# Optimization experiments

Measured on AMD Instinct MI355X. Metric: run time of the kernel, lower is better.

Reference implementation:

```python
import jax, jax.numpy as jnp
import numpy as np

N_WAY = 100
K_SHOT = 10
N_SUPPORT = N_WAY * K_SHOT
N_QUERY = 8192
F_IN = 4096
D_EMB = 1024
EPS = 1e-6  # torch nn.PairwiseDistance default eps added to the difference


def setup_inputs() -> dict:
    key = jax.random.key(0)
    k1, k2, k3, k4 = jax.random.split(key, 4)
    support_images = jax.random.normal(k1, (N_SUPPORT, F_IN), dtype=jnp.float32)
    # dense labels 0..N_WAY-1, K_SHOT examples each (episodic sampling)
    support_labels = (jnp.arange(N_SUPPORT, dtype=jnp.int32) // K_SHOT)
    query_images = jax.random.normal(k2, (N_QUERY, F_IN), dtype=jnp.float32)
    W = jax.random.normal(k3, (F_IN, D_EMB), dtype=jnp.float32) * (1.0 / np.sqrt(F_IN))
    b = jax.random.normal(k4, (D_EMB,), dtype=jnp.float32) * 0.01
    return {"support_images": support_images, "support_labels": support_labels,
            "query_images": query_images, "W": W, "b": b}


def reference(support_images, support_labels, query_images, W, b):
    # backbone: linear feature extractor
    z_support = support_images @ W + b          # [N_SUPPORT, D]
    z_query = query_images @ W + b              # [N_QUERY, D]

    # group support embeddings by class (each class has exactly K_SHOT members)
    order = jnp.argsort(support_labels, stable=True)
    grouped = z_support[order].reshape(N_WAY, K_SHOT, D_EMB)  # [W, K, D]

    # torch .median(dim=0): lower median for even counts -> sorted[(K-1)//2]
    z_proto_med = jnp.sort(grouped, axis=1)[:, (K_SHOT - 1) // 2]  # [W, D]
    z_proto_mean = grouped.mean(axis=1)                            # [W, D]
    z_total = 0.5 * (z_proto_med + z_proto_mean)                   # [W, D]

    # pairwise L2 with torch PairwiseDistance eps: sqrt(sum((q - p + eps)^2))
    # expanded: ||q||^2 + ||p||^2 + D*eps^2 - 2 q.p + 2*eps*(sum q - sum p)
    q2 = jnp.sum(z_query * z_query, axis=-1, keepdims=True)       # [Q, 1]
    p2 = jnp.sum(z_total * z_total, axis=-1)[None, :]             # [1, W]
    qs = jnp.sum(z_query, axis=-1, keepdims=True)                 # [Q, 1]
    ps = jnp.sum(z_total, axis=-1)[None, :]                       # [1, W]
    cross = z_query @ z_total.T                                   # [Q, W]
    sq = q2 + p2 - 2.0 * cross + 2.0 * EPS * (qs - ps) + D_EMB * EPS * EPS
    dists = jnp.sqrt(jnp.maximum(sq, 0.0))                        # [Q, W]
    return -dists
```

## Files before the change

### kernel.cpp

```cpp
#include <hip/hip_runtime.h>


typedef unsigned short u16;
typedef __attribute__((ext_vector_type(4))) unsigned short u16x4;
typedef __attribute__((ext_vector_type(8))) unsigned short u16x8;
typedef __attribute__((ext_vector_type(8))) short bf16x8;
typedef __attribute__((ext_vector_type(4))) float f32x4;

#define N_QUERY 8192
#define F_IN    4096
#define D_EMB   1024
#define N_SUP   1000
#define N_WAY   100
#define BK      64

__device__ __forceinline__ u16 f2b(float f) {
  unsigned int u = __builtin_bit_cast(unsigned int, f);
  u += 0x7FFFu + ((u >> 16) & 1u);
  return (u16)(u >> 16);
}

#define GLB_PTR(p) ((const __attribute__((address_space(1))) unsigned int*)(p))
#define LDS_PTR(p) ((__attribute__((address_space(3))) unsigned int*)(p))

__global__ __launch_bounds__(256) void wt_k(const float* __restrict__ W,
                                            u16* __restrict__ Wt) {
  __shared__ float tile[32][33];
  int kb = blockIdx.x * 32, nb = blockIdx.y * 32;
  int tx = threadIdx.x & 31, ty = threadIdx.x >> 5;
#pragma unroll
  for (int i = 0; i < 4; ++i) {
    int k = ty + i * 8;
    tile[k][tx] = W[(size_t)(kb + k) * D_EMB + nb + tx];
  }
  __syncthreads();
#pragma unroll
  for (int i = 0; i < 4; ++i) {
    int n = ty + i * 8;
    Wt[(size_t)(nb + n) * F_IN + kb + tx] = f2b(tile[tx][n]);
  }
}

__global__ __launch_bounds__(256) void gemm1_k(
    const float* __restrict__ qimg, const float* __restrict__ simg,
    const u16* __restrict__ Wt, const float* __restrict__ bias,
    float* __restrict__ Z) {
  __shared__ __align__(16) u16 As[64 * BK];
  __shared__ __align__(16) u16 Bs[128 * BK];
  const int tid  = threadIdx.x;
  const int lane = tid & 63, wid = tid >> 6;
  const int wr = wid >> 1, wc = wid & 1;
  int lin = blockIdx.x + (blockIdx.y << 3);
  int swz = (lin & 7) * 144 + (lin >> 3);
  const int rowBase = (swz >> 3) * 64;
  const int colBase = (swz & 7) * 128;

  const float* asrc[2];
  int aw[2];
#pragma unroll
  for (int i = 0; i < 2; ++i) {
    int g = i * 256 + tid;
    int row = g >> 3;
    int colb = ((g & 7) << 4) ^ ((row & 7) << 4);
    int grow = rowBase + row;
    int sr = grow - N_QUERY; if (sr < 0) sr = 0; if (sr > N_SUP - 1) sr = N_SUP - 1;
    const float* base = (grow < N_QUERY) ? qimg + (size_t)grow * F_IN
                                         : simg + (size_t)sr * F_IN;
    asrc[i] = base + (colb >> 1);
    aw[i] = g * 8;
  }
  const u16* bsrc[4];
  unsigned bldsoff[4];
#pragma unroll
  for (int i = 0; i < 4; ++i) {
    int g = i * 256 + tid;
    int n = g >> 3;
    int kb = ((g & 7) << 4) ^ ((n & 7) << 4);
    bsrc[i] = Wt + (size_t)(colBase + n) * F_IN + (kb >> 1);
    bldsoff[i] = i * 4096 + wid * 1024;
  }
  int aoff[2], boff[4];
#pragma unroll
  for (int m = 0; m < 2; ++m) {
    int row = wr * 32 + m * 16 + (lane & 15);
    aoff[m] = (row * 128 + (((lane >> 4) << 4) ^ ((row & 7) << 4))) >> 1;
  }
#pragma unroll
  for (int n = 0; n < 4; ++n) {
    int row = wc * 64 + n * 16 + (lane & 15);
    boff[n] = (row * 128 + (((lane >> 4) << 4) ^ ((row & 7) << 4))) >> 1;
  }

  f32x4 acc[2][4] = {};

#pragma unroll 1
  for (int kt = 0; kt < F_IN / BK; ++kt) {
    const float* p0 = asrc[0] + kt * BK;
    const float* p1 = asrc[1] + kt * BK;
    float4 v00 = *(const float4*)p0, v01 = *(const float4*)(p0 + 4);
    float4 v10 = *(const float4*)p1, v11 = *(const float4*)(p1 + 4);
#pragma unroll
    for (int i = 0; i < 4; ++i)
      __builtin_amdgcn_global_load_lds(GLB_PTR(bsrc[i] + kt * BK),
                                       LDS_PTR((char*)Bs + bldsoff[i]), 16, 0, 0);
    u16x8 pk0 = { f2b(v00.x), f2b(v00.y), f2b(v00.z), f2b(v00.w),
                  f2b(v01.x), f2b(v01.y), f2b(v01.z), f2b(v01.w) };
    u16x8 pk1 = { f2b(v10.x), f2b(v10.y), f2b(v10.z), f2b(v10.w),
                  f2b(v11.x), f2b(v11.y), f2b(v11.z), f2b(v11.w) };
    *(u16x8*)&As[aw[0]] = pk0;
    *(u16x8*)&As[aw[1]] = pk1;
    __syncthreads();

#pragma unroll
    for (int ks = 0; ks < 2; ++ks) {
      bf16x8 a[2], b[4];
#pragma unroll
      for (int m = 0; m < 2; ++m) a[m] = *(const bf16x8*)&As[aoff[m] ^ (ks << 5)];
#pragma unroll
      for (int n = 0; n < 4; ++n) b[n] = *(const bf16x8*)&Bs[boff[n] ^ (ks << 5)];
#pragma unroll
      for (int m = 0; m < 2; ++m)
#pragma unroll
        for (int n = 0; n < 4; ++n)
          acc[m][n] = __builtin_amdgcn_mfma_f32_16x16x32_bf16(a[m], b[n], acc[m][n], 0, 0, 0);
    }
    __syncthreads();
  }

#pragma unroll
  for (int n = 0; n < 4; ++n) {
    int c = colBase + wc * 64 + n * 16 + (lane & 15);
    float bvv = bias[c];
#pragma unroll
    for (int m = 0; m < 2; ++m) {
      int r0 = rowBase + wr * 32 + m * 16 + ((lane >> 4) * 4);
#pragma unroll
      for (int r = 0; r < 4; ++r)
        Z[(size_t)(r0 + r) * D_EMB + c] = acc[m][n][r] + bvv;
    }
  }
}

__global__ __launch_bounds__(256) void proto_k(const float* __restrict__ Z,
                                               float* __restrict__ Ztf) {
  int gid = blockIdx.x * 256 + threadIdx.x;
  int w = gid >> 10, d = gid & 1023;
  float outv = 0.f;
  if (w < N_WAY) {
    float v[10]; float s = 0.f;
#pragma unroll
    for (int k = 0; k < 10; ++k) {
      v[k] = Z[(size_t)(N_QUERY + w * 10 + k) * D_EMB + d];
      s += v[k];
    }
#pragma unroll
    for (int a = 0; a < 9; ++a)
#pragma unroll
      for (int b2 = 0; b2 < 9; ++b2)
        if (b2 < 9 - a) {
          float lo = fminf(v[b2], v[b2 + 1]);
          float hi = fmaxf(v[b2], v[b2 + 1]);
          v[b2] = lo; v[b2 + 1] = hi;
        }
    outv = 0.5f * (v[4] + s * 0.1f);
  }
  Ztf[gid] = outv;
}

__global__ __launch_bounds__(256) void stats_k(const float* __restrict__ in,
                                               u16* __restrict__ outb,
                                               float* __restrict__ sum2,
                                               float* __restrict__ sum1) {
  int row = blockIdx.x;
  const float* r = in + (size_t)row * D_EMB;
  int t = threadIdx.x;
  float4 v = *(const float4*)(r + t * 4);
  u16x4 u4 = { f2b(v.x), f2b(v.y), f2b(v.z), f2b(v.w) };
  *(u16x4*)(outb + (size_t)row * D_EMB + t * 4) = u4;
  float s  = v.x + v.y + v.z + v.w;
  float s2 = v.x * v.x + v.y * v.y + v.z * v.z + v.w * v.w;
#pragma unroll
  for (int off = 32; off > 0; off >>= 1) {
    s  += __shfl_down(s, off);
    s2 += __shfl_down(s2, off);
  }
  __shared__ float as1[4], as2[4];
  if ((t & 63) == 0) { as1[t >> 6] = s; as2[t >> 6] = s2; }
  __syncthreads();
  if (t == 0) {
    sum1[row] = as1[0] + as1[1] + as1[2] + as1[3];
    sum2[row] = as2[0] + as2[1] + as2[2] + as2[3];
  }
}

#define LDA2 40
__global__ __launch_bounds__(256) void gemm2_k(
    const u16* __restrict__ Zq, const u16* __restrict__ Ztb,
    const float* __restrict__ q2, const float* __restrict__ qs,
    const float* __restrict__ p2, const float* __restrict__ ps,
    float* __restrict__ out) {
  __shared__ u16 As[64][LDA2];
  __shared__ u16 Bs[128][LDA2];
  const int tid = threadIdx.x;
  const int lane = tid & 63, wid = tid >> 6;
  const int wr = wid >> 1, wc = wid & 1;
  const int rowBase = blockIdx.x * 64;

  f32x4 acc[2][4] = {};

  for (int kt = 0; kt < D_EMB / 32; ++kt) {
    u16x8 avv;
    {
      int row = tid >> 2, kh = tid & 3;
      avv = *(const u16x8*)(Zq + (size_t)(rowBase + row) * D_EMB + kt * 32 + kh * 8);
    }
    u16x8 bvv[2];
#pragma unroll
    for (int i = 0; i < 2; ++i) {
      int u = i * 256 + tid;
      int n = u >> 2, kh = u & 3;
      bvv[i] = *(const u16x8*)(Ztb + (size_t)n * D_EMB + kt * 32 + kh * 8);
    }
    __syncthreads();
    {
      int row = tid >> 2, kh = tid & 3;
      *(u16x8*)&As[row][kh * 8] = avv;
    }
#pragma unroll
    for (int i = 0; i < 2; ++i) {
      int u = i * 256 + tid;
      int n = u >> 2, kh = u & 3;
      *(u16x8*)&Bs[n][kh * 8] = bvv[i];
    }
    __syncthreads();

    bf16x8 a[2], b[4];
#pragma unroll
    for (int m = 0; m < 2; ++m)
      a[m] = *(const bf16x8*)&As[wr * 32 + m * 16 + (lane & 15)][(lane >> 4) * 8];
#pragma unroll
    for (int n = 0; n < 4; ++n)
      b[n] = *(const bf16x8*)&Bs[wc * 64 + n * 16 + (lane & 15)][(lane >> 4) * 8];
#pragma unroll
    for (int m = 0; m < 2; ++m)
#pragma unroll
      for (int n = 0; n < 4; ++n)
        acc[m][n] = __builtin_amdgcn_mfma_f32_16x16x32_bf16(a[m], b[n], acc[m][n], 0, 0, 0);
    __syncthreads();
  }

#pragma unroll
  for (int m = 0; m < 2; ++m) {
    int r0 = rowBase + wr * 32 + m * 16 + ((lane >> 4) * 4);
    float q2v[4], qsv[4];
#pragma unroll
    for (int r = 0; r < 4; ++r) { q2v[r] = q2[r0 + r]; qsv[r] = qs[r0 + r]; }
#pragma unroll
    for (int n = 0; n < 4; ++n) {
      int c = wc * 64 + n * 16 + (lane & 15);
      if (c < N_WAY) {
        float pp = p2[c], pss = ps[c];
#pragma unroll
        for (int r = 0; r < 4; ++r) {
          float sq = q2v[r] + pp - 2.f * acc[m][n][r]
                   + 2e-6f * (qsv[r] - pss) + (float)D_EMB * 1e-12f;
          out[(size_t)(r0 + r) * N_WAY + c] = -sqrtf(fmaxf(sq, 0.f));
        }
      }
    }
  }
}

extern "C" void kernel_launch(void* const* d_in, const int* in_sizes, int n_in,
                              void* d_out, int out_size, void* d_ws, size_t ws_size,
                              hipStream_t stream) {
  const float* simg = (const float*)d_in[0];
  const float* qimg = (const float*)d_in[2];
  const float* W    = (const float*)d_in[3];
  const float* bias = (const float*)d_in[4];
  float* out = (float*)d_out;

  char* ws = (char*)d_ws;
  u16*   Wt  = (u16*)(ws);
  float* Z   = (float*)(ws + 8388608);
  u16*   Zq  = (u16*)(ws + 46137344);
  float* Ztf = (float*)(ws + 62914560);
  u16*   Ztb = (u16*)(ws + 63438848);
  float* q2  = (float*)(ws + 63700992);
  float* qs  = (float*)(ws + 63733760);
  float* p2  = (float*)(ws + 63766528);
  float* ps  = (float*)(ws + 63767040);

  hipLaunchKernelGGL(wt_k,    dim3(128, 32), dim3(256), 0, stream, W, Wt);
  hipLaunchKernelGGL(gemm1_k, dim3(8, 144),  dim3(256), 0, stream, qimg, simg, Wt, bias, Z);
  hipLaunchKernelGGL(proto_k, dim3(512),     dim3(256), 0, stream, Z, Ztf);
  hipLaunchKernelGGL(stats_k, dim3(8192),    dim3(256), 0, stream, Z, Zq, q2, qs);
  hipLaunchKernelGGL(stats_k, dim3(128),     dim3(256), 0, stream, Ztf, Ztb, p2, ps);
  hipLaunchKernelGGL(gemm2_k, dim3(128),     dim3(256), 0, stream, Zq, Ztb, q2, qs, p2, ps, out);
}
```

Baseline: 170.4 us.

## Split GEMM1 K-loop across two warp groups with LDS reduction

```diff
diff --git a/kernel.cpp b/kernel.cpp
--- a/kernel.cpp
+++ b/kernel.cpp
@@ -41,25 +41,29 @@
   }
 }
 
-__global__ __launch_bounds__(256) void gemm1_k(
+__global__ __launch_bounds__(512, 6) void gemm1_k(
     const float* __restrict__ qimg, const float* __restrict__ simg,
     const u16* __restrict__ Wt, const float* __restrict__ bias,
     float* __restrict__ Z) {
-  __shared__ __align__(16) u16 As[64 * BK];
-  __shared__ __align__(16) u16 Bs[128 * BK];
+  __shared__ __align__(16) u16 ldsAll[2][(64 + 128) * BK];
   const int tid  = threadIdx.x;
   const int lane = tid & 63, wid = tid >> 6;
-  const int wr = wid >> 1, wc = wid & 1;
+  const int grp  = wid >> 2, lwid = wid & 3;
+  const int gtid = tid & 255;
+  const int wr = lwid >> 1, wc = lwid & 1;
+  u16* As = &ldsAll[grp][0];
+  u16* Bs = &ldsAll[grp][64 * BK];
   int lin = blockIdx.x + (blockIdx.y << 3);
   int swz = (lin & 7) * 144 + (lin >> 3);
   const int rowBase = (swz >> 3) * 64;
   const int colBase = (swz & 7) * 128;
+  const int kt0 = grp << 5;
 
   const float* asrc[2];
   int aw[2];
 #pragma unroll
   for (int i = 0; i < 2; ++i) {
-    int g = i * 256 + tid;
+    int g = i * 256 + gtid;
     int row = g >> 3;
     int colb = ((g & 7) << 4) ^ ((row & 7) << 4);
     int grow = rowBase + row;
@@ -73,11 +77,11 @@
   unsigned bldsoff[4];
 #pragma unroll
   for (int i = 0; i < 4; ++i) {
-    int g = i * 256 + tid;
+    int g = i * 256 + gtid;
     int n = g >> 3;
     int kb = ((g & 7) << 4) ^ ((n & 7) << 4);
     bsrc[i] = Wt + (size_t)(colBase + n) * F_IN + (kb >> 1);
-    bldsoff[i] = i * 4096 + wid * 1024;
+    bldsoff[i] = i * 4096 + (lwid) * 1024;
   }
   int aoff[2], boff[4];
 #pragma unroll
@@ -94,7 +98,8 @@
   f32x4 acc[2][4] = {};
 
 #pragma unroll 1
-  for (int kt = 0; kt < F_IN / BK; ++kt) {
+  for (int s = 0; s < 32; ++s) {
+    const int kt = kt0 + s;
     const float* p0 = asrc[0] + kt * BK;
     const float* p1 = asrc[1] + kt * BK;
     float4 v00 = *(const float4*)p0, v01 = *(const float4*)(p0 + 4);
@@ -127,16 +132,31 @@
     __syncthreads();
   }
 
-#pragma unroll
-  for (int n = 0; n < 4; ++n) {
-    int c = colBase + wc * 64 + n * 16 + (lane & 15);
-    float bvv = bias[c];
-#pragma unroll
-    for (int m = 0; m < 2; ++m) {
-      int r0 = rowBase + wr * 32 + m * 16 + ((lane >> 4) * 4);
-#pragma unroll
-      for (int r = 0; r < 4; ++r)
-        Z[(size_t)(r0 + r) * D_EMB + c] = acc[m][n][r] + bvv;
+  float* scratch = (float*)&ldsAll[0][0];
+  const int slot = (lwid * 64 + lane) * 32;
+  if (grp == 1) {
+#pragma unroll
+    for (int m = 0; m < 2; ++m)
+#pragma unroll
+      for (int n = 0; n < 4; ++n)
+#pragma unroll
+        for (int r = 0; r < 4; ++r)
+          scratch[slot + (m * 4 + n) * 4 + r] = acc[m][n][r];
+  }
+  __syncthreads();
+  if (grp == 0) {
+#pragma unroll
+    for (int n = 0; n < 4; ++n) {
+      int c = colBase + wc * 64 + n * 16 + (lane & 15);
+      float bvv = bias[c];
+#pragma unroll
+      for (int m = 0; m < 2; ++m) {
+        int r0 = rowBase + wr * 32 + m * 16 + ((lane >> 4) * 4);
+#pragma unroll
+        for (int r = 0; r < 4; ++r)
+          Z[(size_t)(r0 + r) * D_EMB + c] =
+              acc[m][n][r] + scratch[slot + (m * 4 + n) * 4 + r] + bvv;
+      }
     }
   }
 }
@@ -292,7 +312,7 @@
   float* ps  = (float*)(ws + 63767040);
 
   hipLaunchKernelGGL(wt_k,    dim3(128, 32), dim3(256), 0, stream, W, Wt);
-  hipLaunchKernelGGL(gemm1_k, dim3(8, 144),  dim3(256), 0, stream, qimg, simg, Wt, bias, Z);
+  hipLaunchKernelGGL(gemm1_k, dim3(8, 144),  dim3(512), 0, stream, qimg, simg, Wt, bias, Z);
   hipLaunchKernelGGL(proto_k, dim3(512),     dim3(256), 0, stream, Z, Ztf);
   hipLaunchKernelGGL(stats_k, dim3(8192),    dim3(256), 0, stream, Z, Zq, q2, qs);
   hipLaunchKernelGGL(stats_k, dim3(128),     dim3(256), 0, stream, Ztf, Ztb, p2, ps);
```

New measurement: 185.5 us. +8.9%, slower.

## Double-buffer LDS and prefetch A registers two steps ahead in gemm1

Applied to the files above, without the earlier changes.

```diff
diff --git a/kernel.cpp b/kernel.cpp
--- a/kernel.cpp
+++ b/kernel.cpp
@@ -22,6 +22,7 @@
 
 #define GLB_PTR(p) ((const __attribute__((address_space(1))) unsigned int*)(p))
 #define LDS_PTR(p) ((__attribute__((address_space(3))) unsigned int*)(p))
+#define SBAR()  __builtin_amdgcn_sched_barrier(0)
 
 __global__ __launch_bounds__(256) void wt_k(const float* __restrict__ W,
                                             u16* __restrict__ Wt) {
@@ -45,8 +46,8 @@
     const float* __restrict__ qimg, const float* __restrict__ simg,
     const u16* __restrict__ Wt, const float* __restrict__ bias,
     float* __restrict__ Z) {
-  __shared__ __align__(16) u16 As[64 * BK];
-  __shared__ __align__(16) u16 Bs[128 * BK];
+  __shared__ __align__(16) u16 As0[64 * BK],  As1[64 * BK];
+  __shared__ __align__(16) u16 Bs0[128 * BK], Bs1[128 * BK];
   const int tid  = threadIdx.x;
   const int lane = tid & 63, wid = tid >> 6;
   const int wr = wid >> 1, wc = wid & 1;
@@ -92,40 +93,87 @@
   }
 
   f32x4 acc[2][4] = {};
+  float4 aE[2][2], aO[2][2];
+
+#define LOAD_A(REG, KT)                                                        \
+  { const float* p0_ = asrc[0] + (KT) * BK;                                    \
+    const float* p1_ = asrc[1] + (KT) * BK;                                    \
+    REG[0][0] = *(const float4*)p0_; REG[0][1] = *(const float4*)(p0_ + 4);    \
+    REG[1][0] = *(const float4*)p1_; REG[1][1] = *(const float4*)(p1_ + 4); }
+
+#define STAGE_B(DST, KT)                                                       \
+  { _Pragma("unroll")                                                          \
+    for (int i_ = 0; i_ < 4; ++i_)                                             \
+      __builtin_amdgcn_global_load_lds(GLB_PTR(bsrc[i_] + (KT) * BK),          \
+          LDS_PTR((char*)(DST) + bldsoff[i_]), 16, 0, 0); }
+
+#define CVT_A(DST, REG)                                                        \
+  { u16x8 pk0_ = { f2b(REG[0][0].x), f2b(REG[0][0].y), f2b(REG[0][0].z),       \
+                   f2b(REG[0][0].w), f2b(REG[0][1].x), f2b(REG[0][1].y),       \
+                   f2b(REG[0][1].z), f2b(REG[0][1].w) };                       \
+    u16x8 pk1_ = { f2b(REG[1][0].x), f2b(REG[1][0].y), f2b(REG[1][0].z),       \
+                   f2b(REG[1][0].w), f2b(REG[1][1].x), f2b(REG[1][1].y),       \
+                   f2b(REG[1][1].z), f2b(REG[1][1].w) };                       \
+    *(u16x8*)&(DST)[aw[0]] = pk0_;                                             \
+    *(u16x8*)&(DST)[aw[1]] = pk1_; }
+
+#define COMPUTE(CURA, CURB)                                                    \
+  { _Pragma("unroll")                                                          \
+    for (int ks = 0; ks < 2; ++ks) {                                           \
+      bf16x8 a_[2], b_[4];                                                     \
+      _Pragma("unroll")                                                        \
+      for (int m = 0; m < 2; ++m)                                              \
+        a_[m] = *(const bf16x8*)&(CURA)[aoff[m] ^ (ks << 5)];                  \
+      _Pragma("unroll")                                                        \
+      for (int n = 0; n < 4; ++n)                                              \
+        b_[n] = *(const bf16x8*)&(CURB)[boff[n] ^ (ks << 5)];                  \
+      _Pragma("unroll")                                                        \
+      for (int m = 0; m < 2; ++m)                                              \
+        _Pragma("unroll")                                                      \
+        for (int n = 0; n < 4; ++n)                                            \
+          acc[m][n] = __builtin_amdgcn_mfma_f32_16x16x32_bf16(a_[m], b_[n],    \
+                                                              acc[m][n], 0, 0, 0); } }
+
+#define STEP(T, KT2, CURA, CURB, NXTA, NXTB, RC, RN)                           \
+  {                                                                            \
+    STAGE_B(NXTB, (T) + 1);                                                    \
+    SBAR();                                                                    \
+    LOAD_A(RN, KT2);                                                           \
+    SBAR();                                                                    \
+    COMPUTE(CURA, CURB);                                                       \
+    CVT_A(NXTA, RC);                                                           \
+    asm volatile("s_waitcnt vmcnt(4) lgkmcnt(0)" ::: "memory");                \
+    SBAR();                                                                    \
+    __builtin_amdgcn_s_barrier();                                              \
+    SBAR();                                                                    \
+  }
+
+  STAGE_B(Bs0, 0);
+  SBAR();
+  LOAD_A(aE, 0);
+  SBAR();
+  LOAD_A(aO, 1);
+  SBAR();
+  CVT_A(As0, aE);
+  asm volatile("s_waitcnt vmcnt(4) lgkmcnt(0)" ::: "memory");
+  SBAR();
+  __builtin_amdgcn_s_barrier();
+  SBAR();
 
 #pragma unroll 1
-  for (int kt = 0; kt < F_IN / BK; ++kt) {
-    const float* p0 = asrc[0] + kt * BK;
-    const float* p1 = asrc[1] + kt * BK;
-    float4 v00 = *(const float4*)p0, v01 = *(const float4*)(p0 + 4);
-    float4 v10 = *(const float4*)p1, v11 = *(const float4*)(p1 + 4);
-#pragma unroll
-    for (int i = 0; i < 4; ++i)
-      __builtin_amdgcn_global_load_lds(GLB_PTR(bsrc[i] + kt * BK),
-                                       LDS_PTR((char*)Bs + bldsoff[i]), 16, 0, 0);
-    u16x8 pk0 = { f2b(v00.x), f2b(v00.y), f2b(v00.z), f2b(v00.w),
-                  f2b(v01.x), f2b(v01.y), f2b(v01.z), f2b(v01.w) };
-    u16x8 pk1 = { f2b(v10.x), f2b(v10.y), f2b(v10.z), f2b(v10.w),
-                  f2b(v11.x), f2b(v11.y), f2b(v11.z), f2b(v11.w) };
-    *(u16x8*)&As[aw[0]] = pk0;
-    *(u16x8*)&As[aw[1]] = pk1;
-    __syncthreads();
-
-#pragma unroll
-    for (int ks = 0; ks < 2; ++ks) {
-      bf16x8 a[2], b[4];
-#pragma unroll
-      for (int m = 0; m < 2; ++m) a[m] = *(const bf16x8*)&As[aoff[m] ^ (ks << 5)];
-#pragma unroll
-      for (int n = 0; n < 4; ++n) b[n] = *(const bf16x8*)&Bs[boff[n] ^ (ks << 5)];
-#pragma unroll
-      for (int m = 0; m < 2; ++m)
-#pragma unroll
-        for (int n = 0; n < 4; ++n)
-          acc[m][n] = __builtin_amdgcn_mfma_f32_16x16x32_bf16(a[m], b[n], acc[m][n], 0, 0, 0);
-    }
-    __syncthreads();
-  }
+  for (int t2 = 0; t2 < 31; ++t2) {
+    const int t = 2 * t2;
+    STEP(t,     t + 2, As0, Bs0, As1, Bs1, aO, aE);
+    STEP(t + 1, t + 3, As1, Bs1, As0, Bs0, aE, aO);
+  }
+  STEP(62, 63, As0, Bs0, As1, Bs1, aO, aE);
+  COMPUTE(As1, Bs1);
+
+#undef STEP
+#undef COMPUTE
+#undef CVT_A
+#undef STAGE_B
+#undef LOAD_A
 
 #pragma unroll
   for (int n = 0; n < 4; ++n) {
```

Result: slower. 197.1 us (+15.7%).

## Pre-convert query images to bf16 and emit bf16 embeddings from the first GEMM

Applied to the files above, without the earlier changes.

```diff
diff --git a/kernel.cpp b/kernel.cpp
--- a/kernel.cpp
+++ b/kernel.cpp
@@ -19,6 +19,10 @@
   u += 0x7FFFu + ((u >> 16) & 1u);
   return (u16)(u >> 16);
 }
+__device__ __forceinline__ float b2f(u16 u) {
+  unsigned int x = ((unsigned int)u) << 16;
+  return __builtin_bit_cast(float, x);
+}
 
 #define GLB_PTR(p) ((const __attribute__((address_space(1))) unsigned int*)(p))
 #define LDS_PTR(p) ((__attribute__((address_space(3))) unsigned int*)(p))
@@ -41,10 +45,20 @@
   }
 }
 
+__global__ __launch_bounds__(256) void acvt_k(const float* __restrict__ qimg,
+                                              u16* __restrict__ Ab) {
+  size_t i = ((size_t)blockIdx.x * 256 + threadIdx.x) * 8;
+  float4 v0 = *(const float4*)(qimg + i);
+  float4 v1 = *(const float4*)(qimg + i + 4);
+  u16x8 pk = { f2b(v0.x), f2b(v0.y), f2b(v0.z), f2b(v0.w),
+               f2b(v1.x), f2b(v1.y), f2b(v1.z), f2b(v1.w) };
+  *(u16x8*)(Ab + i) = pk;
+}
+
 __global__ __launch_bounds__(256) void gemm1_k(
-    const float* __restrict__ qimg, const float* __restrict__ simg,
+    const u16* __restrict__ Ab, const float* __restrict__ simg,
     const u16* __restrict__ Wt, const float* __restrict__ bias,
-    float* __restrict__ Z) {
+    u16* __restrict__ Zq) {
   __shared__ __align__(16) u16 As[64 * BK];
   __shared__ __align__(16) u16 Bs[128 * BK];
   const int tid  = threadIdx.x;
@@ -54,20 +68,23 @@
   int swz = (lin & 7) * 144 + (lin >> 3);
   const int rowBase = (swz >> 3) * 64;
   const int colBase = (swz & 7) * 128;
-
-  const float* asrc[2];
+  const bool pure = (rowBase < N_QUERY);
+
+  const u16*   asrcP[2];
+  const float* asrcS[2];
   int aw[2];
+  unsigned aldsoff[2];
 #pragma unroll
   for (int i = 0; i < 2; ++i) {
     int g = i * 256 + tid;
     int row = g >> 3;
     int colb = ((g & 7) << 4) ^ ((row & 7) << 4);
     int grow = rowBase + row;
+    asrcP[i] = Ab + (size_t)(grow < N_QUERY ? grow : 0) * F_IN + (colb >> 1);
     int sr = grow - N_QUERY; if (sr < 0) sr = 0; if (sr > N_SUP - 1) sr = N_SUP - 1;
-    const float* base = (grow < N_QUERY) ? qimg + (size_t)grow * F_IN
-                                         : simg + (size_t)sr * F_IN;
-    asrc[i] = base + (colb >> 1);
+    asrcS[i] = simg + (size_t)sr * F_IN + (colb >> 1);
     aw[i] = g * 8;
+    aldsoff[i] = i * 4096 + wid * 1024;
   }
   const u16* bsrc[4];
   unsigned bldsoff[4];
@@ -93,39 +110,61 @@
 
   f32x4 acc[2][4] = {};
 
+#define COMPUTE()                                                              \
+  { _Pragma("unroll")                                                          \
+    for (int ks = 0; ks < 2; ++ks) {                                           \
+      bf16x8 a_[2], b_[4];                                                     \
+      _Pragma("unroll")                                                        \
+      for (int m = 0; m < 2; ++m)                                              \
+        a_[m] = *(const bf16x8*)&As[aoff[m] ^ (ks << 5)];                      \
+      _Pragma("unroll")                                                        \
+      for (int n = 0; n < 4; ++n)                                              \
+        b_[n] = *(const bf16x8*)&Bs[boff[n] ^ (ks << 5)];                      \
+      _Pragma("unroll")                                                        \
+      for (int m = 0; m < 2; ++m)                                              \
+        _Pragma("unroll")                                                      \
+        for (int n = 0; n < 4; ++n)                                            \
+          acc[m][n] = __builtin_amdgcn_mfma_f32_16x16x32_bf16(a_[m], b_[n],    \
+                                                              acc[m][n], 0, 0, 0); } }
+
+  if (pure) {
 #pragma unroll 1
-  for (int kt = 0; kt < F_IN / BK; ++kt) {
-    const float* p0 = asrc[0] + kt * BK;
-    const float* p1 = asrc[1] + kt * BK;
-    float4 v00 = *(const float4*)p0, v01 = *(const float4*)(p0 + 4);
-    float4 v10 = *(const float4*)p1, v11 = *(const float4*)(p1 + 4);
-#pragma unroll
-    for (int i = 0; i < 4; ++i)
-      __builtin_amdgcn_global_load_lds(GLB_PTR(bsrc[i] + kt * BK),
-                                       LDS_PTR((char*)Bs + bldsoff[i]), 16, 0, 0);
-    u16x8 pk0 = { f2b(v00.x), f2b(v00.y), f2b(v00.z), f2b(v00.w),
-                  f2b(v01.x), f2b(v01.y), f2b(v01.z), f2b(v01.w) };
-    u16x8 pk1 = { f2b(v10.x), f2b(v10.y), f2b(v10.z), f2b(v10.w),
-                  f2b(v11.x), f2b(v11.y), f2b(v11.z), f2b(v11.w) };
-    *(u16x8*)&As[aw[0]] = pk0;
-    *(u16x8*)&As[aw[1]] = pk1;
-    __syncthreads();
-
-#pragma unroll
-    for (int ks = 0; ks < 2; ++ks) {
-      bf16x8 a[2], b[4];
-#pragma unroll
-      for (int m = 0; m < 2; ++m) a[m] = *(const bf16x8*)&As[aoff[m] ^ (ks << 5)];
-#pragma unroll
-      for (int n = 0; n < 4; ++n) b[n] = *(const bf16x8*)&Bs[boff[n] ^ (ks << 5)];
-#pragma unroll
-      for (int m = 0; m < 2; ++m)
-#pragma unroll
-        for (int n = 0; n < 4; ++n)
-          acc[m][n] = __builtin_amdgcn_mfma_f32_16x16x32_bf16(a[m], b[n], acc[m][n], 0, 0, 0);
-    }
-    __syncthreads();
-  }
+    for (int kt = 0; kt < F_IN / BK; ++kt) {
+#pragma unroll
+      for (int i = 0; i < 2; ++i)
+        __builtin_amdgcn_global_load_lds(GLB_PTR(asrcP[i] + kt * BK),
+                                         LDS_PTR((char*)As + aldsoff[i]), 16, 0, 0);
+#pragma unroll
+      for (int i = 0; i < 4; ++i)
+        __builtin_amdgcn_global_load_lds(GLB_PTR(bsrc[i] + kt * BK),
+                                         LDS_PTR((char*)Bs + bldsoff[i]), 16, 0, 0);
+      __syncthreads();
+      COMPUTE();
+      __syncthreads();
+    }
+  } else {
+#pragma unroll 1
+    for (int kt = 0; kt < F_IN / BK; ++kt) {
+      const float* p0 = asrcS[0] + kt * BK;
+      const float* p1 = asrcS[1] + kt * BK;
+      float4 v00 = *(const float4*)p0, v01 = *(const float4*)(p0 + 4);
+      float4 v10 = *(const float4*)p1, v11 = *(const float4*)(p1 + 4);
+#pragma unroll
+      for (int i = 0; i < 4; ++i)
+        __builtin_amdgcn_global_load_lds(GLB_PTR(bsrc[i] + kt * BK),
+                                         LDS_PTR((char*)Bs + bldsoff[i]), 16, 0, 0);
+      u16x8 pk0 = { f2b(v00.x), f2b(v00.y), f2b(v00.z), f2b(v00.w),
+                    f2b(v01.x), f2b(v01.y), f2b(v01.z), f2b(v01.w) };
+      u16x8 pk1 = { f2b(v10.x), f2b(v10.y), f2b(v10.z), f2b(v10.w),
+                    f2b(v11.x), f2b(v11.y), f2b(v11.z), f2b(v11.w) };
+      *(u16x8*)&As[aw[0]] = pk0;
+      *(u16x8*)&As[aw[1]] = pk1;
+      __syncthreads();
+      COMPUTE();
+      __syncthreads();
+    }
+  }
+#undef COMPUTE
 
 #pragma unroll
   for (int n = 0; n < 4; ++n) {
@@ -136,12 +175,12 @@
       int r0 = rowBase + wr * 32 + m * 16 + ((lane >> 4) * 4);
 #pragma unroll
       for (int r = 0; r < 4; ++r)
-        Z[(size_t)(r0 + r) * D_EMB + c] = acc[m][n][r] + bvv;
-    }
-  }
-}
-
-__global__ __launch_bounds__(256) void proto_k(const float* __restrict__ Z,
+        Zq[(size_t)(r0 + r) * D_EMB + c] = f2b(acc[m][n][r] + bvv);
+    }
+  }
+}
+
+__global__ __launch_bounds__(256) void proto_k(const u16* __restrict__ Zq,
                                                float* __restrict__ Ztf) {
   int gid = blockIdx.x * 256 + threadIdx.x;
   int w = gid >> 10, d = gid & 1023;
@@ -150,7 +189,7 @@
     float v[10]; float s = 0.f;
 #pragma unroll
     for (int k = 0; k < 10; ++k) {
-      v[k] = Z[(size_t)(N_QUERY + w * 10 + k) * D_EMB + d];
+      v[k] = b2f(Zq[(size_t)(N_QUERY + w * 10 + k) * D_EMB + d]);
       s += v[k];
     }
 #pragma unroll
@@ -165,6 +204,29 @@
     outv = 0.5f * (v[4] + s * 0.1f);
   }
   Ztf[gid] = outv;
+}
+
+__global__ __launch_bounds__(256) void statsq_k(const u16* __restrict__ Zq,
+                                                float* __restrict__ sum2,
+                                                float* __restrict__ sum1) {
+  int row = blockIdx.x;
+  int t = threadIdx.x;
+  u16x4 u = *(const u16x4*)(Zq + (size_t)row * D_EMB + t * 4);
+  float x0 = b2f(u[0]), x1 = b2f(u[1]), x2 = b2f(u[2]), x3 = b2f(u[3]);
+  float s  = x0 + x1 + x2 + x3;
+  float s2 = x0 * x0 + x1 * x1 + x2 * x2 + x3 * x3;
+#pragma unroll
+  for (int o = 32; o > 0; o >>= 1) {
+    s  += __shfl_down(s, o);
+    s2 += __shfl_down(s2, o);
+  }
+  __shared__ float as1[4], as2[4];
+  if ((t & 63) == 0) { as1[t >> 6] = s; as2[t >> 6] = s2; }
+  __syncthreads();
+  if (t == 0) {
+    sum1[row] = as1[0] + as1[1] + as1[2] + as1[3];
+    sum2[row] = as2[0] + as2[1] + as2[2] + as2[3];
+  }
 }
 
 __global__ __launch_bounds__(256) void stats_k(const float* __restrict__ in,
@@ -282,19 +344,20 @@
 
   char* ws = (char*)d_ws;
   u16*   Wt  = (u16*)(ws);
-  float* Z   = (float*)(ws + 8388608);
-  u16*   Zq  = (u16*)(ws + 46137344);
-  float* Ztf = (float*)(ws + 62914560);
-  u16*   Ztb = (u16*)(ws + 63438848);
-  float* q2  = (float*)(ws + 63700992);
-  float* qs  = (float*)(ws + 63733760);
-  float* p2  = (float*)(ws + 63766528);
-  float* ps  = (float*)(ws + 63767040);
+  u16*   Ab  = (u16*)(ws + 8388608);
+  u16*   Zq  = (u16*)(ws + 75497472);
+  float* Ztf = (float*)(ws + 94371840);
+  u16*   Ztb = (u16*)(ws + 94896128);
+  float* q2  = (float*)(ws + 95158272);
+  float* qs  = (float*)(ws + 95191040);
+  float* p2  = (float*)(ws + 95223808);
+  float* ps  = (float*)(ws + 95224320);
 
   hipLaunchKernelGGL(wt_k,    dim3(128, 32), dim3(256), 0, stream, W, Wt);
-  hipLaunchKernelGGL(gemm1_k, dim3(8, 144),  dim3(256), 0, stream, qimg, simg, Wt, bias, Z);
-  hipLaunchKernelGGL(proto_k, dim3(512),     dim3(256), 0, stream, Z, Ztf);
-  hipLaunchKernelGGL(stats_k, dim3(8192),    dim3(256), 0, stream, Z, Zq, q2, qs);
+  hipLaunchKernelGGL(acvt_k,  dim3(16384),   dim3(256), 0, stream, qimg, Ab);
+  hipLaunchKernelGGL(gemm1_k, dim3(8, 144),  dim3(256), 0, stream, Ab, simg, Wt, bias, Zq);
+  hipLaunchKernelGGL(proto_k, dim3(512),     dim3(256), 0, stream, Zq, Ztf);
+  hipLaunchKernelGGL(statsq_k, dim3(8192),   dim3(256), 0, stream, Zq, q2, qs);
   hipLaunchKernelGGL(stats_k, dim3(128),     dim3(256), 0, stream, Ztf, Ztb, p2, ps);
   hipLaunchKernelGGL(gemm2_k, dim3(128),     dim3(256), 0, stream, Zq, Ztb, q2, qs, p2, ps, out);
 }
```

Result: slower. 208.4 us (+22.3%).
